# Kernel tuning notes

Measured on AMD Instinct MI355X. Metric: run time of the kernel, lower is better.

Reference implementation:

```python
import jax, jax.numpy as jnp
import numpy as np

EMBED = 1024
NUM_EXPERTS = 8
ACTIVE = 2
HIDDEN = 4 * EMBED


def setup_inputs() -> dict:
    key = jax.random.key(0)
    ks = jax.random.split(key, 7)
    B, T = 4, 1024
    s1 = 1.0 / np.sqrt(EMBED)
    s2 = 1.0 / np.sqrt(HIDDEN)
    return {
        "x": jax.random.normal(ks[0], (B, T, EMBED), dtype=jnp.float32),
        # stacked expert weights, layout [in, out] (torch Linear applies x @ W.T + b)
        "W1": jax.random.uniform(ks[1], (NUM_EXPERTS, EMBED, HIDDEN), jnp.float32, -s1, s1),
        "b1": jax.random.uniform(ks[2], (NUM_EXPERTS, HIDDEN), jnp.float32, -s1, s1),
        "W2": jax.random.uniform(ks[3], (NUM_EXPERTS, HIDDEN, EMBED), jnp.float32, -s2, s2),
        "b2": jax.random.uniform(ks[4], (NUM_EXPERTS, EMBED), jnp.float32, -s2, s2),
        "Wr": jax.random.uniform(ks[5], (EMBED, NUM_EXPERTS), jnp.float32, -s1, s1),
        "br": jax.random.uniform(ks[6], (NUM_EXPERTS,), jnp.float32, -s1, s1),
    }


def reference(x, W1, b1, W2, b2, Wr, br):
    # ---- router (TopkRouter) ----
    scores = x @ Wr + br                                  # [B,T,E]
    topk_scores, indices = jax.lax.top_k(scores, ACTIVE)  # [B,T,K]
    # mask = zeros scattered with topk scores at topk positions (others stay 0),
    # then softmax over ALL experts (faithful to the reference's quirky softmax).
    one_hot = jax.nn.one_hot(indices, NUM_EXPERTS, dtype=scores.dtype)  # [B,T,K,E]
    mask = jnp.einsum('btke,btk->bte', one_hot, topk_scores)            # [B,T,E]
    router_output = jax.nn.softmax(mask, axis=-1)                       # [B,T,E]

    # ---- dense all-experts FFN (Expert): relu(x@W1+b1)@W2+b2 per expert ----
    h = jax.nn.relu(jnp.einsum('btd,edh->bteh', x, W1) + b1)            # [B,T,E,H]
    expert_outputs = jnp.einsum('bteh,ehd->bted', h, W2) + b2           # [B,T,E,D]

    # ---- weighted combine ----
    return jnp.einsum('bte,bted->btd', router_output, expert_outputs)   # [B,T,D]
```

## Files before the change

kernel.cpp:

```cpp
#include <hip/hip_runtime.h>
#include <hip/hip_bf16.h>
#include <cstdint>
#include <cstddef>

#define EMBED  1024
#define NEXP   8
#define HIDDEN 4096
#define TOKENS 4096

typedef __attribute__((ext_vector_type(8))) short bf16x8;
typedef __attribute__((ext_vector_type(4))) float f32x4;
using bf16 = __hip_bfloat16;

__device__ __forceinline__ void gload_lds16(const void* g, void* l) {
    __builtin_amdgcn_global_load_lds((const __attribute__((address_space(1))) void*)g,
                                     (__attribute__((address_space(3))) void*)l,
                                     16, 0, 0);
}

__device__ __forceinline__ int swz(int b) { return b ^ (((b >> 7) & 7) << 4); }

__global__ void cvt_kernel(const float* __restrict__ in, bf16* __restrict__ out, size_t n) {
    size_t i = ((size_t)blockIdx.x * blockDim.x + threadIdx.x) * 4;
    if (i + 3 < n) {
        float4 v = *(const float4*)(in + i);
        out[i + 0] = __float2bfloat16(v.x);
        out[i + 1] = __float2bfloat16(v.y);
        out[i + 2] = __float2bfloat16(v.z);
        out[i + 3] = __float2bfloat16(v.w);
    }
}

__global__ void transpose_cvt(const float* __restrict__ in, bf16* __restrict__ out,
                              int K, int N, size_t in_estride, size_t out_eoff, int ldo) {
    const int e = blockIdx.z;
    const float* ine = in + (size_t)e * in_estride;
    bf16* oute = out + (size_t)e * out_eoff;
    __shared__ float tile[32][33];
    const int n0 = blockIdx.x * 32, k0 = blockIdx.y * 32;
    const int tx = threadIdx.x, ty = threadIdx.y;
    #pragma unroll
    for (int i = ty; i < 32; i += 8)
        tile[i][tx] = ine[(size_t)(k0 + i) * N + n0 + tx];
    __syncthreads();
    #pragma unroll
    for (int i = ty; i < 32; i += 8)
        oute[(size_t)(n0 + i) * ldo + k0 + tx] = __float2bfloat16(tile[tx][i]);
}

__global__ void router_kernel(const float* __restrict__ x, const float* __restrict__ Wr,
                              const float* __restrict__ br, float* __restrict__ w) {
    const int t = blockIdx.x;
    const int lane = threadIdx.x;
    const float* xt = x + (size_t)t * EMBED;
    float s[NEXP];
    #pragma unroll
    for (int e = 0; e < NEXP; e++) s[e] = 0.f;
    for (int k = lane; k < EMBED; k += 64) {
        const float xv = xt[k];
        const float* wrk = Wr + (size_t)k * NEXP;
        #pragma unroll
        for (int e = 0; e < NEXP; e++) s[e] = fmaf(xv, wrk[e], s[e]);
    }
    #pragma unroll
    for (int e = 0; e < NEXP; e++) {
        #pragma unroll
        for (int off = 32; off >= 1; off >>= 1)
            s[e] += __shfl_xor(s[e], off);
    }
    if (lane == 0) {
        float sc[NEXP];
        #pragma unroll
        for (int e = 0; e < NEXP; e++) sc[e] = s[e] + br[e];
        int i1 = 0; float m1 = sc[0];
        #pragma unroll
        for (int e = 1; e < NEXP; e++) if (sc[e] > m1) { m1 = sc[e]; i1 = e; }
        int i2 = -1; float m2 = -1e30f;
        #pragma unroll
        for (int e = 0; e < NEXP; e++) if (e != i1 && sc[e] > m2) { m2 = sc[e]; i2 = e; }
        const float mx = fmaxf(m1, 0.f);
        const float denom = 6.f * expf(0.f - mx) + expf(m1 - mx) + expf(m2 - mx);
        #pragma unroll
        for (int e = 0; e < NEXP; e++) {
            float v = (e == i1) ? m1 : ((e == i2) ? m2 : 0.f);
            w[(size_t)t * NEXP + e] = expf(v - mx) / denom;
        }
    }
}

__global__ __launch_bounds__(256) void gemm1(const bf16* __restrict__ A,
                                             const bf16* __restrict__ Bt,
                                             const float* __restrict__ b1,
                                             const float* __restrict__ rw,
                                             bf16* __restrict__ H) {
    const int e = blockIdx.z;
    const int brow = blockIdx.y * 128;
    const int bcol = blockIdx.x * 128;
    const bf16* Be = Bt + (size_t)e * HIDDEN * EMBED;
    bf16* He = H + (size_t)e * TOKENS * HIDDEN;
    __shared__ __align__(16) bf16 As[128 * 32];
    __shared__ __align__(16) bf16 Bs[128 * 32];
    const int tid = threadIdx.x;
    f32x4 acc[4][4] = {};

    const int seg0 = tid, seg1 = tid + 256;
    const int r0 = seg0 >> 2, c0 = seg0 & 3;
    const int r1 = seg1 >> 2, c1 = seg1 & 3;
    const bf16* ga0 = A + (size_t)(brow + r0) * EMBED + c0 * 8;
    const bf16* ga1 = A + (size_t)(brow + r1) * EMBED + c1 * 8;
    const bf16* gb0 = Be + (size_t)(bcol + r0) * EMBED + c0 * 8;
    const bf16* gb1 = Be + (size_t)(bcol + r1) * EMBED + c1 * 8;

    const int lane = tid & 63, wid = tid >> 6;
    const int wv_r = (wid >> 1) * 64, wv_c = (wid & 1) * 64;
    const int fr = lane & 15, kb = (lane >> 4) * 8;

    for (int kt = 0; kt < EMBED; kt += 32) {
        gload_lds16(ga0 + kt, As + seg0 * 8);
        gload_lds16(ga1 + kt, As + seg1 * 8);
        gload_lds16(gb0 + kt, Bs + seg0 * 8);
        gload_lds16(gb1 + kt, Bs + seg1 * 8);
        __syncthreads();
        bf16x8 af[4], bfr[4];
        #pragma unroll
        for (int m = 0; m < 4; m++) af[m] = *(const bf16x8*)&As[(wv_r + m * 16 + fr) * 32 + kb];
        #pragma unroll
        for (int n = 0; n < 4; n++) bfr[n] = *(const bf16x8*)&Bs[(wv_c + n * 16 + fr) * 32 + kb];
        #pragma unroll
        for (int m = 0; m < 4; m++)
            #pragma unroll
            for (int n = 0; n < 4; n++)
                acc[m][n] = __builtin_amdgcn_mfma_f32_16x16x32_bf16(af[m], bfr[n], acc[m][n], 0, 0, 0);
        __syncthreads();
    }

    #pragma unroll
    for (int n = 0; n < 4; n++) {
        const int col = bcol + wv_c + n * 16 + fr;
        const float bias = b1[e * HIDDEN + col];
        #pragma unroll
        for (int m = 0; m < 4; m++) {
            const int rowb = brow + wv_r + m * 16 + (lane >> 4) * 4;
            #pragma unroll
            for (int j = 0; j < 4; j++) {
                const int row = rowb + j;
                float v = acc[m][n][j] + bias;
                v = fmaxf(v, 0.f) * rw[(size_t)row * NEXP + e];
                He[(size_t)row * HIDDEN + col] = __float2bfloat16(v);
            }
        }
    }
}


#define BARX()  { __builtin_amdgcn_sched_barrier(0); __builtin_amdgcn_s_barrier(); __builtin_amdgcn_sched_barrier(0); }
#define LGKM0() { asm volatile("s_waitcnt lgkmcnt(0)" ::: "memory"); __builtin_amdgcn_sched_barrier(0); }

#define PIPE_PREAMBLE(Abase, Bbase, lda, ldb)                                        \
    __shared__ __align__(16) bf16 As[2][2][128 * 64];                                \
    __shared__ __align__(16) bf16 Bs[2][2][128 * 64];                                \
    const int tid = threadIdx.x;                                                     \
    const int lane = tid & 63, wid = tid >> 6;                                       \
    const int mhalf = wid >> 2, wB = wid & 3;                                        \
    const int nhalf = wB >> 1, nsub = wB & 1;                                        \
    const int wv_r = mhalf * 128, wv_c = wB * 64;                                    \
    f32x4 acc[8][4] = {};                                                            \
    int rowloc[2], colel[2];                                                         \
    _Pragma("unroll")                                                                \
    for (int j = 0; j < 2; j++) {                                                    \
        int bs = swz(tid * 16 + j * 8192);                                           \
        rowloc[j] = bs >> 7; colel[j] = (bs & 127) >> 1;                             \
    }                                                                                \
    const bf16* pA0 = (Abase) + (size_t)(brow + rowloc[0]) * (lda) + colel[0];       \
    const bf16* pA1 = (Abase) + (size_t)(brow + rowloc[1]) * (lda) + colel[1];       \
    const bf16* pB0 = (Bbase) + (size_t)(bcol + rowloc[0]) * (ldb) + colel[0];       \
    const bf16* pB1 = (Bbase) + (size_t)(bcol + rowloc[1]) * (ldb) + colel[1];       \
    const int fr = lane & 15, kb0 = (lane >> 4) * 16;                                \
    const int xm = (fr & 7) << 4;                                                    \
    const int baA0 = (fr * 128 + kb0) ^ xm, baA1 = (fr * 128 + kb0 + 64) ^ xm;       \
    const int brB = (nsub * 64 + fr) * 128;                                          \
    const int baB0 = (brB + kb0) ^ xm, baB1 = (brB + kb0 + 64) ^ xm;

#define STAGE_A(bi, h, koff, lda)                                                    \
    do {                                                                             \
        gload_lds16(pA0 + (size_t)(h) * 128 * (lda) + (koff), &As[bi][h][tid * 8]);  \
        gload_lds16(pA1 + (size_t)(h) * 128 * (lda) + (koff), &As[bi][h][tid * 8 + 4096]); \
    } while (0)
#define STAGE_B(bi, h, koff, ldb)                                                    \
    do {                                                                             \
        gload_lds16(pB0 + (size_t)(h) * 128 * (ldb) + (koff), &Bs[bi][h][tid * 8]);  \
        gload_lds16(pB1 + (size_t)(h) * 128 * (ldb) + (koff), &Bs[bi][h][tid * 8 + 4096]); \
    } while (0)

#define MFMA_Q(mh, nh)                                                               \
    __builtin_amdgcn_s_setprio(1);                                                   \
    _Pragma("unroll")                                                                \
    for (int mm = 0; mm < 4; mm++)                                                   \
        _Pragma("unroll")                                                            \
        for (int nn = 0; nn < 2; nn++) {                                             \
            acc[(mh)*4+mm][(nh)*2+nn] = __builtin_amdgcn_mfma_f32_16x16x32_bf16(     \
                a[(mh)*4+mm][0], b[(nh)*2+nn][0], acc[(mh)*4+mm][(nh)*2+nn], 0,0,0); \
            acc[(mh)*4+mm][(nh)*2+nn] = __builtin_amdgcn_mfma_f32_16x16x32_bf16(     \
                a[(mh)*4+mm][1], b[(nh)*2+nn][1], acc[(mh)*4+mm][(nh)*2+nn], 0,0,0); \
        }                                                                            \
    __builtin_amdgcn_s_setprio(0);

#define PIPE_KLOOP(NT, lda, ldb)                                                     \
    STAGE_A(0, 0, 0, lda); STAGE_A(0, 1, 0, lda);                                    \
    STAGE_B(0, 0, 0, ldb); STAGE_B(0, 1, 0, ldb);                                    \
    STAGE_A(1, 0, 64, lda); STAGE_A(1, 1, 64, lda);                                  \
    STAGE_B(1, 0, 64, ldb); STAGE_B(1, 1, 64, ldb);                                  \
    asm volatile("s_waitcnt vmcnt(8)" ::: "memory");                                 \
    BARX();                                                                          \
    for (int t = 0; t < (NT); ++t) {                                                 \
        const int bi = t & 1;                                                        \
        const bool st = (t + 2) < (NT);                                              \
        const size_t koff = (size_t)(t + 2) * 64;                                    \
        const char* Ah = (const char*)&As[bi][mhalf][0];                             \
        const char* Bh = (const char*)&Bs[bi][nhalf][0];                             \
        bf16x8 a[8][2], b[4][2];                                                     \
                                        \
        _Pragma("unroll")                                                            \
        for (int m = 0; m < 4; m++) {                                                \
            a[m][0] = *(const bf16x8*)(Ah + baA0 + m * 2048);                        \
            a[m][1] = *(const bf16x8*)(Ah + baA1 + m * 2048);                        \
        }                                                                            \
        _Pragma("unroll")                                                            \
        for (int n = 0; n < 2; n++) {                                                \
            b[n][0] = *(const bf16x8*)(Bh + baB0 + n * 2048);                        \
            b[n][1] = *(const bf16x8*)(Bh + baB1 + n * 2048);                        \
        }                                                                            \
        BARX(); LGKM0();                                                             \
        MFMA_Q(0, 0)                                                                 \
             \
        _Pragma("unroll")                                                            \
        for (int n = 2; n < 4; n++) {                                                \
            b[n][0] = *(const bf16x8*)(Bh + baB0 + n * 2048);                        \
            b[n][1] = *(const bf16x8*)(Bh + baB1 + n * 2048);                        \
        }                                                                            \
        BARX(); LGKM0();                                                             \
        MFMA_Q(0, 1)                                                                 \
        BARX();                                                                      \
           \
        _Pragma("unroll")                                                            \
        for (int m = 4; m < 8; m++) {                                                \
            a[m][0] = *(const bf16x8*)(Ah + baA0 + m * 2048);                        \
            a[m][1] = *(const bf16x8*)(Ah + baA1 + m * 2048);                        \
        }                                                                            \
        if (st) { STAGE_B(bi, 0, koff, ldb); STAGE_B(bi, 1, koff, ldb); }            \
        BARX(); LGKM0();                                                             \
        MFMA_Q(1, 0)                                                                 \
        BARX();                                                                      \
             \
        if (st) { STAGE_A(bi, 0, koff, lda); STAGE_A(bi, 1, koff, lda); }            \
        MFMA_Q(1, 1)                                                                 \
        if (st) { asm volatile("s_waitcnt vmcnt(8)" ::: "memory"); }                 \
        else    { asm volatile("s_waitcnt vmcnt(0)" ::: "memory"); }                 \
        BARX();                                                                      \
    }

__global__ __launch_bounds__(512, 2) void gemm2(const bf16* __restrict__ A,
                                                const bf16* __restrict__ Bt,
                                                const float* __restrict__ b2,
                                                const float* __restrict__ rw,
                                                float* __restrict__ out) {
    const int e = blockIdx.z;
    const int brow = blockIdx.y * 256;
    const int bcol = blockIdx.x * 256;
    const bf16* Ae = A + (size_t)e * TOKENS * HIDDEN;
    const bf16* Be = Bt + (size_t)e * EMBED * HIDDEN;

    PIPE_PREAMBLE(Ae, Be, HIDDEN, HIDDEN)
    PIPE_KLOOP(64, HIDDEN, HIDDEN)

    #pragma unroll
    for (int n = 0; n < 4; n++) {
        const int col = bcol + wv_c + n * 16 + fr;
        #pragma unroll
        for (int m = 0; m < 8; m++) {
            const int rowb = brow + wv_r + m * 16 + (lane >> 4) * 4;
            #pragma unroll
            for (int j = 0; j < 4; j++) {
                const int row = rowb + j;
                float v = acc[m][n][j];
                if (e == 0) {
                    const float* wrow = rw + (size_t)row * NEXP;
                    float s = 0.f;
                    #pragma unroll
                    for (int ee = 0; ee < NEXP; ee++) s = fmaf(wrow[ee], b2[ee * EMBED + col], s);
                    v += s;
                }
                atomicAdd(out + (size_t)row * EMBED + col, v);
            }
        }
    }
}

extern "C" void kernel_launch(void* const* d_in, const int* in_sizes, int n_in,
                              void* d_out, int out_size, void* d_ws, size_t ws_size,
                              hipStream_t stream) {
    const float* x  = (const float*)d_in[0];
    const float* W1 = (const float*)d_in[1];
    const float* b1 = (const float*)d_in[2];
    const float* W2 = (const float*)d_in[3];
    const float* b2 = (const float*)d_in[4];
    const float* Wr = (const float*)d_in[5];
    const float* br = (const float*)d_in[6];
    float* out = (float*)d_out;

    uint8_t* ws = (uint8_t*)d_ws;
    size_t off = 0;
    auto walloc = [&](size_t bytes) -> void* {
        void* p = ws + off;
        off += (bytes + 255) & ~(size_t)255;
        return p;
    };
    float* rw  = (float*)walloc((size_t)TOKENS * NEXP * 4);
    bf16* xb   = (bf16*)walloc((size_t)TOKENS * EMBED * 2);
    bf16* w1t  = (bf16*)walloc((size_t)NEXP * HIDDEN * EMBED * 2);
    bf16* w2t  = (bf16*)walloc((size_t)NEXP * EMBED * HIDDEN * 2);
    bf16* hbuf = (bf16*)walloc((size_t)NEXP * TOKENS * HIDDEN * 2);

    hipMemsetAsync(d_out, 0, (size_t)out_size * sizeof(float), stream);

    cvt_kernel<<<4096, 256, 0, stream>>>(x, xb, (size_t)TOKENS * EMBED);

    dim3 tb(32, 8);
    transpose_cvt<<<dim3(HIDDEN / 32, EMBED / 32, NEXP), tb, 0, stream>>>(
        W1, w1t, EMBED, HIDDEN, (size_t)EMBED * HIDDEN, (size_t)HIDDEN * EMBED, EMBED);
    transpose_cvt<<<dim3(EMBED / 32, HIDDEN / 32, NEXP), tb, 0, stream>>>(
        W2, w2t, HIDDEN, EMBED, (size_t)HIDDEN * EMBED, (size_t)EMBED * HIDDEN, HIDDEN);

    router_kernel<<<TOKENS, 64, 0, stream>>>(x, Wr, br, rw);

    gemm1<<<dim3(HIDDEN / 128, TOKENS / 128, NEXP), 256, 0, stream>>>(xb, w1t, b1, rw, hbuf);
    gemm2<<<dim3(EMBED / 256, TOKENS / 256, NEXP), 512, 0, stream>>>(hbuf, w2t, b2, rw, out);
}
```

Measured before the change: 941.5 us.

## Chunk gemm1 by tokens and merge expert pairs in gemm2 K-loop

```diff
diff --git a/kernel.cpp b/kernel.cpp
--- a/kernel.cpp
+++ b/kernel.cpp
@@ -7,6 +7,7 @@
 #define NEXP   8
 #define HIDDEN 4096
 #define TOKENS 4096
+#define MC     1024
 
 typedef __attribute__((ext_vector_type(8))) short bf16x8;
 typedef __attribute__((ext_vector_type(4))) float f32x4;
@@ -18,7 +19,7 @@
                                      16, 0, 0);
 }
 
-__device__ __forceinline__ int swz(int b) { return b ^ (((b >> 7) & 7) << 4); }
+__device__ __forceinline__ int swzB(int b) { return b ^ (((b >> 7) & 7) << 4); }
 
 __global__ void cvt_kernel(const float* __restrict__ in, bf16* __restrict__ out, size_t n) {
     size_t i = ((size_t)blockIdx.x * blockDim.x + threadIdx.x) * 4;
@@ -97,7 +98,7 @@
     const int brow = blockIdx.y * 128;
     const int bcol = blockIdx.x * 128;
     const bf16* Be = Bt + (size_t)e * HIDDEN * EMBED;
-    bf16* He = H + (size_t)e * TOKENS * HIDDEN;
+    bf16* He = H + (size_t)e * MC * HIDDEN;
     __shared__ __align__(16) bf16 As[128 * 32];
     __shared__ __align__(16) bf16 Bs[128 * 32];
     const int tid = threadIdx.x;
@@ -152,9 +153,10 @@
     }
 }
 
-
 #define BARX()  { __builtin_amdgcn_sched_barrier(0); __builtin_amdgcn_s_barrier(); __builtin_amdgcn_sched_barrier(0); }
 #define LGKM0() { asm volatile("s_waitcnt lgkmcnt(0)" ::: "memory"); __builtin_amdgcn_sched_barrier(0); }
+
+#define KOFF(T, estride) ((size_t)((T) & 63) * 64 + (size_t)((T) >> 6) * (estride))
 
 #define PIPE_PREAMBLE(Abase, Bbase, lda, ldb)                                        \
     __shared__ __align__(16) bf16 As[2][2][128 * 64];                                \
@@ -168,7 +170,7 @@
     int rowloc[2], colel[2];                                                         \
     _Pragma("unroll")                                                                \
     for (int j = 0; j < 2; j++) {                                                    \
-        int bs = swz(tid * 16 + j * 8192);                                           \
+        int bs = swzB(tid * 16 + j * 8192);                                          \
         rowloc[j] = bs >> 7; colel[j] = (bs & 127) >> 1;                             \
     }                                                                                \
     const bf16* pA0 = (Abase) + (size_t)(brow + rowloc[0]) * (lda) + colel[0];       \
@@ -205,7 +207,7 @@
         }                                                                            \
     __builtin_amdgcn_s_setprio(0);
 
-#define PIPE_KLOOP(NT, lda, ldb)                                                     \
+#define PIPE_KLOOP(NT, lda, ldb, eA, eB)                                             \
     STAGE_A(0, 0, 0, lda); STAGE_A(0, 1, 0, lda);                                    \
     STAGE_B(0, 0, 0, ldb); STAGE_B(0, 1, 0, ldb);                                    \
     STAGE_A(1, 0, 64, lda); STAGE_A(1, 1, 64, lda);                                  \
@@ -215,7 +217,8 @@
     for (int t = 0; t < (NT); ++t) {                                                 \
         const int bi = t & 1;                                                        \
         const bool st = (t + 2) < (NT);                                              \
-        const size_t koff = (size_t)(t + 2) * 64;                                    \
+        const size_t koffA = KOFF(t + 2, eA);                                        \
+        const size_t koffB = KOFF(t + 2, eB);                                        \
         const char* Ah = (const char*)&As[bi][mhalf][0];                             \
         const char* Bh = (const char*)&Bs[bi][nhalf][0];                             \
         bf16x8 a[8][2], b[4][2];                                                     \
@@ -232,7 +235,7 @@
         }                                                                            \
         BARX(); LGKM0();                                                             \
         MFMA_Q(0, 0)                                                                 \
-             \
+                                                   \
         _Pragma("unroll")                                                            \
         for (int n = 2; n < 4; n++) {                                                \
             b[n][0] = *(const bf16x8*)(Bh + baB0 + n * 2048);                        \
@@ -241,18 +244,18 @@
         BARX(); LGKM0();                                                             \
         MFMA_Q(0, 1)                                                                 \
         BARX();                                                                      \
-           \
+                                     \
         _Pragma("unroll")                                                            \
         for (int m = 4; m < 8; m++) {                                                \
             a[m][0] = *(const bf16x8*)(Ah + baA0 + m * 2048);                        \
             a[m][1] = *(const bf16x8*)(Ah + baA1 + m * 2048);                        \
         }                                                                            \
-        if (st) { STAGE_B(bi, 0, koff, ldb); STAGE_B(bi, 1, koff, ldb); }            \
+        if (st) { STAGE_B(bi, 0, koffB, ldb); STAGE_B(bi, 1, koffB, ldb); }          \
         BARX(); LGKM0();                                                             \
         MFMA_Q(1, 0)                                                                 \
         BARX();                                                                      \
-             \
-        if (st) { STAGE_A(bi, 0, koff, lda); STAGE_A(bi, 1, koff, lda); }            \
+                       \
+        if (st) { STAGE_A(bi, 0, koffA, lda); STAGE_A(bi, 1, koffA, lda); }          \
         MFMA_Q(1, 1)                                                                 \
         if (st) { asm volatile("s_waitcnt vmcnt(8)" ::: "memory"); }                 \
         else    { asm volatile("s_waitcnt vmcnt(0)" ::: "memory"); }                 \
@@ -264,26 +267,30 @@
                                                 const float* __restrict__ b2,
                                                 const float* __restrict__ rw,
                                                 float* __restrict__ out) {
-    const int e = blockIdx.z;
-    const int brow = blockIdx.y * 256;
+    const int kc = blockIdx.z;
+    const int brow_g = blockIdx.y * 256;
     const int bcol = blockIdx.x * 256;
-    const bf16* Ae = A + (size_t)e * TOKENS * HIDDEN;
-    const bf16* Be = Bt + (size_t)e * EMBED * HIDDEN;
+    const size_t eAc = (size_t)MC * HIDDEN;
+    const size_t CHST = (size_t)NEXP * MC * HIDDEN;
+    const size_t eB = (size_t)EMBED * HIDDEN;
+    const bf16* Ae = A + (size_t)(brow_g >> 10) * CHST + (size_t)(kc * 2) * eAc;
+    const bf16* Be = Bt + (size_t)(kc * 2) * eB;
+    const int brow = brow_g & (MC - 1);
 
     PIPE_PREAMBLE(Ae, Be, HIDDEN, HIDDEN)
-    PIPE_KLOOP(64, HIDDEN, HIDDEN)
+    PIPE_KLOOP(128, HIDDEN, HIDDEN, eAc, eB)
 
     #pragma unroll
     for (int n = 0; n < 4; n++) {
         const int col = bcol + wv_c + n * 16 + fr;
         #pragma unroll
         for (int m = 0; m < 8; m++) {
-            const int rowb = brow + wv_r + m * 16 + (lane >> 4) * 4;
+            const int rowb = brow_g + wv_r + m * 16 + (lane >> 4) * 4;
             #pragma unroll
             for (int j = 0; j < 4; j++) {
                 const int row = rowb + j;
                 float v = acc[m][n][j];
-                if (e == 0) {
+                if (kc == 0) {
                     const float* wrow = rw + (size_t)row * NEXP;
                     float s = 0.f;
                     #pragma unroll
@@ -333,6 +340,11 @@
 
     router_kernel<<<TOKENS, 64, 0, stream>>>(x, Wr, br, rw);
 
-    gemm1<<<dim3(HIDDEN / 128, TOKENS / 128, NEXP), 256, 0, stream>>>(xb, w1t, b1, rw, hbuf);
-    gemm2<<<dim3(EMBED / 256, TOKENS / 256, NEXP), 512, 0, stream>>>(hbuf, w2t, b2, rw, out);
-}
+    const size_t CHST = (size_t)NEXP * MC * HIDDEN;
+    for (int c = 0; c < TOKENS / MC; ++c) {
+        gemm1<<<dim3(HIDDEN / 128, MC / 128, NEXP), 256, 0, stream>>>(
+            xb + (size_t)c * MC * EMBED, w1t, b1, rw + (size_t)c * MC * NEXP,
+            hbuf + (size_t)c * CHST);
+    }
+    gemm2<<<dim3(EMBED / 256, TOKENS / 256, 4), 512, 0, stream>>>(hbuf, w2t, b2, rw, out);
+}
```

Result: faster. 901.0 us (-4.3%).
